# Kernel tuning notes

Measured on AMD Instinct MI355X. Metric: run time of the kernel, lower is better.

Reference implementation:

```python
import jax, jax.numpy as jnp
import numpy as np

N, M = 50000, 12
ORIG, NBR_F, AF = 92, 41, 64
B, NA = 500, 100
NCONV = 3
BN_EPS = 1e-5


def _batchnorm(x, g, b):
    # training-mode batchnorm over axis 0 (biased variance, like torch)
    mu = jnp.mean(x, axis=0)
    var = jnp.mean((x - mu) ** 2, axis=0)
    return (x - mu) * jax.lax.rsqrt(var + BN_EPS) * g + b


def _conv_layer(atom, nbr_fea, nbr_idx, W, bW, g1, b1, g2, b2):
    n, m = nbr_idx.shape
    atom_nbr = atom[nbr_idx]                                   # [N,M,AF] gather
    center = jnp.broadcast_to(atom[:, None, :], (n, m, AF))
    total = jnp.concatenate([center, atom_nbr, nbr_fea], axis=2)  # [N,M,2AF+NBR_F]
    gated = jnp.einsum('nmf,of->nmo', total, W) + bW              # [N,M,2AF]
    gated = _batchnorm(gated.reshape(-1, 2 * AF), g1, b1).reshape(n, m, 2 * AF)
    filt, core = gated[..., :AF], gated[..., AF:]
    summed = jnp.sum(jax.nn.sigmoid(filt) * jax.nn.softplus(core), axis=1)  # [N,AF]
    summed = _batchnorm(summed, g2, b2)
    return jax.nn.softplus(atom + summed)


def setup_inputs() -> dict:
    key = jax.random.key(0)
    ks = jax.random.split(key, 12)
    inp = {
        'atom_fea': jax.random.normal(ks[0], (N, ORIG), jnp.float32),
        'nbr_fea': jax.random.normal(ks[1], (N, M, NBR_F), jnp.float32),
        'nbr_fea_idx': jax.random.randint(ks[2], (N, M), 0, N, jnp.int32),
        'crystal_atom_idx': jnp.arange(B * NA, dtype=jnp.int32).reshape(B, NA),
        'mask': jnp.ones((ORIG,), jnp.float32),
        'emb_W': jax.random.normal(ks[3], (AF, ORIG), jnp.float32) * 0.05,
        'conv_W': jax.random.normal(ks[4], (NCONV, 2 * AF, 2 * AF + NBR_F), jnp.float32) * 0.05,
        'conv_b': jnp.zeros((NCONV, 2 * AF), jnp.float32),
        'bn1_g': jnp.ones((NCONV, 2 * AF), jnp.float32),
        'bn1_b': jnp.zeros((NCONV, 2 * AF), jnp.float32),
        'bn2_g': jnp.ones((NCONV, AF), jnp.float32),
        'bn2_b': jnp.zeros((NCONV, AF), jnp.float32),
        'fc1_W': jax.random.normal(ks[5], (AF, AF), jnp.float32) * 0.05,
        'fc1_b': jnp.zeros((AF,), jnp.float32),
        'fc2_W': jax.random.normal(ks[6], (AF, AF), jnp.float32) * 0.05,
        'fc2_b': jnp.zeros((AF,), jnp.float32),
        'out_W': jax.random.normal(ks[7], (1, AF), jnp.float32) * 0.05,
        'out_b': jnp.zeros((1,), jnp.float32),
    }
    return inp


def reference(atom_fea, nbr_fea, nbr_fea_idx, crystal_atom_idx, mask, emb_W,
              conv_W, conv_b, bn1_g, bn1_b, bn2_g, bn2_b,
              fc1_W, fc1_b, fc2_W, fc2_b, out_W, out_b):
    x = atom_fea * mask                      # learned input mask
    atom_mask_feature = x
    h = x @ emb_W.T                          # embedding, no bias -> [N,AF]
    for i in range(NCONV):
        h = _conv_layer(h, nbr_fea, nbr_fea_idx, conv_W[i], conv_b[i],
                        bn1_g[i], bn1_b[i], bn2_g[i], bn2_b[i])
    g = h[crystal_atom_idx]                  # [B,NA,AF]
    norm = jnp.sqrt(jnp.sum(g * g, axis=-1, keepdims=True))
    g = g / jnp.maximum(norm, 1e-12)         # F.normalize p=2
    pooled = jnp.mean(g, axis=1)             # [B,AF]
    z = jax.nn.softplus(pooled @ fc1_W.T + fc1_b)
    z = jax.nn.softplus(z @ fc2_W.T + fc2_b)
    props = z @ out_W.T + out_b              # [B,1]
    return props, atom_mask_feature
```

## Files before the change

kernel.cpp:

```cpp
#include <hip/hip_runtime.h>
#include <hip/hip_bf16.h>
#include <stdint.h>

#define NN      50000
#define MMN     12
#define NMROWS  600000
#define ORIGF   92
#define NBRF    41
#define AFD     64
#define GCH     128
#define KTOT    169
#define BBC     500
#define NAA     100
#define BN_EPS  1e-5f
#define GROWS   96

typedef unsigned short u16;
typedef __attribute__((ext_vector_type(8))) short bf16x8;
typedef __attribute__((ext_vector_type(4))) float f32x4;

__device__ __forceinline__ float b2f(u16 u) {
    union { uint32_t i; float f; } v; v.i = ((uint32_t)u) << 16; return v.f;
}
__device__ __forceinline__ float hi2f(uint32_t p) {
    union { uint32_t i; float f; } v; v.i = p & 0xffff0000u; return v.f;
}
__device__ __forceinline__ u16 f2b(float f) {
    __hip_bfloat16 h = __float2bfloat16(f);
    return *(u16*)&h;
}
__device__ __forceinline__ float sp_f(float x) {
    return fmaxf(x, 0.f) + __logf(1.f + __expf(-fabsf(x)));
}
__device__ __forceinline__ float sigm_f(float x) {
    return __builtin_amdgcn_rcpf(1.f + __expf(-x));
}

__global__ void k_mask(const float* __restrict__ atom, const float* __restrict__ mask,
                       float* __restrict__ dout) {
    int i = blockIdx.x * blockDim.x + threadIdx.x;
    int stride = gridDim.x * blockDim.x;
    for (; i < NN * ORIGF; i += stride) {
        int k = i % ORIGF;
        dout[BBC + i] = atom[i] * mask[k];
    }
}

__global__ __launch_bounds__(256, 2) void k_emb(const float* __restrict__ atom,
                                                const float* __restrict__ mask,
                                                const float* __restrict__ embW,
                                                u16* __restrict__ h) {
    __shared__ float xs[4 * 96];
    int lane = threadIdx.x & 63;
    int w = threadIdx.x >> 6;
    float wr[ORIGF];
#pragma unroll
    for (int k = 0; k < ORIGF; ++k) wr[k] = embW[lane * ORIGF + k];
    float m1 = mask[lane];
    float m2 = (lane < ORIGF - 64) ? mask[64 + lane] : 0.f;
    for (int base = blockIdx.x * 4; base < NN; base += gridDim.x * 4) {
        int n = base + w;
        xs[w * 96 + lane] = atom[(size_t)n * ORIGF + lane] * m1;
        if (lane < ORIGF - 64)
            xs[w * 96 + 64 + lane] = atom[(size_t)n * ORIGF + 64 + lane] * m2;
        __syncthreads();
        float acc = 0.f;
#pragma unroll
        for (int k4 = 0; k4 < ORIGF / 4; ++k4) {
            float4 f = *(const float4*)&xs[w * 96 + 4 * k4];
            acc += f.x * wr[4*k4] + f.y * wr[4*k4+1] + f.z * wr[4*k4+2] + f.w * wr[4*k4+3];
        }
        h[(size_t)n * AFD + lane] = f2b(acc);
        __syncthreads();
    }
}

__global__ __launch_bounds__(256, 2) void k_cn(const u16* __restrict__ h,
                                               const float* __restrict__ convW,
                                               uint32_t* __restrict__ C32) {
    __shared__ float xs[2 * AFD];
    int lane = threadIdx.x & 63;
    int w = threadIdx.x >> 6;
    int half = w & 1;
    int sub = w >> 1;
    int koff = half * AFD;
    float wa[AFD], wb[AFD];
#pragma unroll
    for (int k = 0; k < AFD; ++k) {
        wa[k] = convW[lane * KTOT + koff + k];
        wb[k] = convW[(lane + 64) * KTOT + koff + k];
    }
    for (int base = blockIdx.x * 2; base < NN; base += gridDim.x * 2) {
        int n = base + sub;
        if (half == 0) xs[sub * AFD + lane] = b2f(h[(size_t)n * AFD + lane]);
        __syncthreads();
        float aa = 0.f, ab = 0.f;
#pragma unroll
        for (int k4 = 0; k4 < AFD / 4; ++k4) {
            float4 f = *(const float4*)&xs[sub * AFD + 4 * k4];
            aa += f.x * wa[4*k4] + f.y * wa[4*k4+1] + f.z * wa[4*k4+2] + f.w * wa[4*k4+3];
            ab += f.x * wb[4*k4] + f.y * wb[4*k4+1] + f.z * wb[4*k4+2] + f.w * wb[4*k4+3];
        }
        C32[(size_t)n * 128 + half * 64 + lane] = (uint32_t)f2b(aa) | ((uint32_t)f2b(ab) << 16);
        __syncthreads();
    }
}

__device__ __forceinline__ void stage_nbrf(const float* nbrf, int r0, float* fs) {
    const float4* src = (const float4*)(nbrf + (size_t)r0 * NBRF);
    for (int t = threadIdx.x; t < (GROWS * NBRF) / 4; t += 256) {
        float4 f = src[t];
        float vals[4] = {f.x, f.y, f.z, f.w};
#pragma unroll
        for (int j = 0; j < 4; ++j) {
            int e = t * 4 + j;
            int row = e / NBRF;
            int k = e - row * NBRF;
            fs[row * 44 + k] = vals[j];
        }
    }
}

template<bool STORE>
__global__ __launch_bounds__(256, 4) void k_gs4(
    const uint32_t* __restrict__ C32, const float* __restrict__ nbrf,
    const int* __restrict__ nbridx, const float* __restrict__ convW,
    const float* __restrict__ convb, float* __restrict__ stats,
    uint32_t* __restrict__ gated32)
{
    __shared__ __align__(16) u16 As[GROWS * 56];
    __shared__ uint32_t C2s[GROWS * 65];
    __shared__ uint32_t C1s[8 * 65];
    const int tid  = threadIdx.x;
    const int lane = tid & 63;
    const int w    = tid >> 6;
    const int lr   = lane & 15;
    const int lg   = lane >> 4;
    const int r0    = blockIdx.x * GROWS;
    const int nbase = blockIdx.x * (GROWS / MMN);
    const int rowb  = w * 24;

    uint32_t c2v[12];
#pragma unroll
    for (int rr = 0; rr < 12; ++rr) {
        int j = nbridx[r0 + rowb + rr];
        c2v[rr] = C32[(size_t)j * 128 + 64 + lane];
    }
    uint32_t c1v[2];
#pragma unroll
    for (int q = 0; q < 2; ++q) {
        int e = tid + q * 256;
        c1v[q] = C32[(size_t)(nbase + (e >> 6)) * 128 + (e & 63)];
    }
    const float4* src4 = (const float4*)(nbrf + (size_t)r0 * NBRF);
#pragma unroll
    for (int it = 0; it < 4; ++it) {
        int t = tid + it * 256;
        if (it < 3 || t < 984) {
            float4 f = src4[t];
            float vals[4] = {f.x, f.y, f.z, f.w};
#pragma unroll
            for (int jj = 0; jj < 4; ++jj) {
                int e = t * 4 + jj;
                int row = e / NBRF;
                int k = e - row * NBRF;
                As[row * 56 + k] = f2b(vals[jj]);
            }
        }
    }
#pragma unroll
    for (int rr = 0; rr < 12; ++rr) C2s[(rowb + rr) * 65 + lane] = c2v[rr];
#pragma unroll
    for (int rr = 0; rr < 12; ++rr) {
        int j = nbridx[r0 + rowb + 12 + rr];
        c2v[rr] = C32[(size_t)j * 128 + 64 + lane];
    }
#pragma unroll
    for (int q = 0; q < 2; ++q) {
        int e = tid + q * 256;
        C1s[(e >> 6) * 65 + (e & 63)] = c1v[q];
    }
#pragma unroll
    for (int it = 0; it < 6; ++it) {
        int e = tid + it * 256;
        if (it < 5 || e < 1440) {
            int row = e / 15;
            int k = 41 + (e - row * 15);
            As[row * 56 + k] = (k == 41) ? (u16)0x3F80 : (u16)0;
        }
    }
    const int chlo = w * 16 + lr;
    const int chhi = chlo + 64;
    const float* wlo = convW + (size_t)chlo * KTOT + 128;
    const float* whi = convW + (size_t)chhi * KTOT + 128;
    bf16x8 bl0, bh0;
    bf16x8 bl1 = {0,0,0,0,0,0,0,0}, bh1 = {0,0,0,0,0,0,0,0};
#pragma unroll
    for (int e = 0; e < 8; ++e) {
        bl0[e] = (short)f2b(wlo[8 * lg + e]);
        bh0[e] = (short)f2b(whi[8 * lg + e]);
    }
    if (lg == 0) {
#pragma unroll
        for (int e = 0; e < 8; ++e) {
            bl1[e] = (short)f2b(wlo[32 + e]);
            bh1[e] = (short)f2b(whi[32 + e]);
        }
    } else if (lg == 1) {
        bl1[0] = (short)f2b(wlo[40]); bl1[1] = (short)f2b(convb[chlo]);
        bh1[0] = (short)f2b(whi[40]); bh1[1] = (short)f2b(convb[chhi]);
    }
#pragma unroll
    for (int rr = 0; rr < 12; ++rr) C2s[(rowb + 12 + rr) * 65 + lane] = c2v[rr];
    __syncthreads();

    f32x4 acc[6][2];
    const f32x4 z = {0.f, 0.f, 0.f, 0.f};
    const bf16x8 zb = {0,0,0,0,0,0,0,0};
#pragma unroll
    for (int mt = 0; mt < 6; ++mt) {
        const u16* ap = &As[(mt * 16 + lr) * 56 + 8 * lg];
        bf16x8 a0 = *(const bf16x8*)ap;
        bf16x8 a1 = zb;
        if (lg < 3) a1 = *(const bf16x8*)(ap + 32);
        acc[mt][0] = __builtin_amdgcn_mfma_f32_16x16x32_bf16(a1, bl1,
                     __builtin_amdgcn_mfma_f32_16x16x32_bf16(a0, bl0, z, 0, 0, 0), 0, 0, 0);
        acc[mt][1] = __builtin_amdgcn_mfma_f32_16x16x32_bf16(a1, bh1,
                     __builtin_amdgcn_mfma_f32_16x16x32_bf16(a0, bh0, z, 0, 0, 0), 0, 0, 0);
    }

    const int word = w * 16 + lr;
    float slo = 0.f, qlo = 0.f, shi = 0.f, qhi = 0.f;
#pragma unroll
    for (int mt = 0; mt < 6; ++mt) {
#pragma unroll
        for (int rg = 0; rg < 4; ++rg) {
            int row = mt * 16 + 4 * lg + rg;
            uint32_t p1 = C1s[(row / MMN) * 65 + word];
            uint32_t p2 = C2s[row * 65 + word];
            float glo = acc[mt][0][rg] + b2f((u16)p1) + b2f((u16)p2);
            float ghi = acc[mt][1][rg] + hi2f(p1) + hi2f(p2);
            if (STORE) {
                gated32[(size_t)(r0 + row) * 64 + word] =
                    (uint32_t)f2b(glo) | ((uint32_t)f2b(ghi) << 16);
            }
            slo += glo; qlo = fmaf(glo, glo, qlo);
            shi += ghi; qhi = fmaf(ghi, ghi, qhi);
        }
    }
    slo += __shfl_xor(slo, 16, 64); slo += __shfl_xor(slo, 32, 64);
    qlo += __shfl_xor(qlo, 16, 64); qlo += __shfl_xor(qlo, 32, 64);
    shi += __shfl_xor(shi, 16, 64); shi += __shfl_xor(shi, 32, 64);
    qhi += __shfl_xor(qhi, 16, 64); qhi += __shfl_xor(qhi, 32, 64);
    if (lane < 16) {
        atomicAdd(&stats[word], slo);
        atomicAdd(&stats[128 + word], qlo);
        atomicAdd(&stats[64 + word], shi);
        atomicAdd(&stats[128 + 64 + word], qhi);
    }
}

__global__ void k_fin(float* __restrict__ stats, const float* __restrict__ gg,
                      const float* __restrict__ bb, int nch, float invcnt,
                      int sumoff, int sqoff, int scoff, int shoff) {
    int c = threadIdx.x;
    if (c < nch) {
        float mean = stats[sumoff + c] * invcnt;
        float var  = fmaxf(stats[sqoff + c] * invcnt - mean * mean, 0.f);
        float sc   = gg[c] * rsqrtf(var + BN_EPS);
        stats[scoff + c] = sc;
        stats[shoff + c] = bb[c] - mean * sc;
    }
}

__global__ __launch_bounds__(256) void k_acts(
    const uint32_t* __restrict__ gated32, float* __restrict__ stats,
    u16* __restrict__ summed)
{
    __shared__ float red[4][64][2];
    int lane = threadIdx.x & 63;
    int w = threadIdx.x >> 6;
    float sa = stats[384 + lane],      ba = stats[512 + lane];
    float sb = stats[384 + 64 + lane], bb = stats[512 + 64 + lane];
    int wave = blockIdx.x * 4 + w, nw = gridDim.x * 4;
    float s2 = 0.f, q2 = 0.f;
    for (int n = wave; n < NN; n += nw) {
        const uint32_t* gr = gated32 + (size_t)n * MMN * 64;
        float s = 0.f;
#pragma unroll
        for (int m = 0; m < MMN; ++m) {
            uint32_t p = gr[m * 64 + lane];
            float f1 = b2f((u16)p) * sa + ba;
            float cc = hi2f(p) * sb + bb;
            s += sigm_f(f1) * sp_f(cc);
        }
        summed[(size_t)n * AFD + lane] = f2b(s);
        s2 += s; q2 += s * s;
    }
    red[w][lane][0] = s2; red[w][lane][1] = q2;
    __syncthreads();
    if (threadIdx.x < 64) {
        int c = threadIdx.x;
        float a = 0, b = 0;
#pragma unroll
        for (int ww = 0; ww < 4; ++ww) { a += red[ww][c][0]; b += red[ww][c][1]; }
        atomicAdd(&stats[256 + c], a);
        atomicAdd(&stats[320 + c], b);
    }
}

__device__ __forceinline__ void edge_dot(const float* fr, const float* wfa,
                                         const float* wfb, float& aa, float& ab) {
#pragma unroll
    for (int k4 = 0; k4 < 10; ++k4) {
        float4 f = *(const float4*)&fr[4 * k4];
        aa += f.x * wfa[4*k4] + f.y * wfa[4*k4+1] + f.z * wfa[4*k4+2] + f.w * wfa[4*k4+3];
        ab += f.x * wfb[4*k4] + f.y * wfb[4*k4+1] + f.z * wfb[4*k4+2] + f.w * wfb[4*k4+3];
    }
    aa += fr[40] * wfa[40];
    ab += fr[40] * wfb[40];
}

__global__ __launch_bounds__(256) void k_act(
    const uint32_t* __restrict__ C32, const float* __restrict__ nbrf,
    const int* __restrict__ nbridx, const float* __restrict__ convW,
    const float* __restrict__ convb, float* __restrict__ stats,
    u16* __restrict__ summed)
{
    __shared__ float fs[GROWS * 44];
    __shared__ float red[4][64][2];
    int lane = threadIdx.x & 63;
    int w = threadIdx.x >> 6;
    int r0 = blockIdx.x * GROWS;
    stage_nbrf(nbrf, r0, fs);
    float wfa[NBRF], wfb[NBRF];
#pragma unroll
    for (int k = 0; k < NBRF; ++k) {
        wfa[k] = convW[lane * KTOT + 128 + k];
        wfb[k] = convW[(lane + 64) * KTOT + 128 + k];
    }
    float biasa = convb[lane], biasb = convb[64 + lane];
    float sa = stats[384 + lane],      ba = stats[512 + lane];
    float sb = stats[384 + 64 + lane], bb = stats[512 + 64 + lane];
    __syncthreads();
    float s2 = 0.f, q2 = 0.f;
    float s = 0.f;
    float c1a = 0.f, c1b = 0.f;
    for (int rr = 0; rr < 24; ++rr) {
        int rl = w * 24 + rr;
        int r = r0 + rl;
        if ((rr % MMN) == 0) {
            int n = r / MMN;
            uint32_t p1 = C32[(size_t)n * 128 + lane];
            c1a = b2f((u16)p1); c1b = b2f((u16)(p1 >> 16));
            s = 0.f;
        }
        int j = nbridx[r];
        uint32_t p2 = C32[(size_t)j * 128 + 64 + lane];
        float aa = c1a + b2f((u16)p2) + biasa;
        float ab = c1b + b2f((u16)(p2 >> 16)) + biasb;
        edge_dot(&fs[rl * 44], wfa, wfb, aa, ab);
        float f1 = aa * sa + ba;
        float cc = ab * sb + bb;
        s += sigm_f(f1) * sp_f(cc);
        if ((rr % MMN) == MMN - 1) {
            int n = r / MMN;
            summed[(size_t)n * AFD + lane] = f2b(s);
            s2 += s; q2 += s * s;
        }
    }
    red[w][lane][0] = s2; red[w][lane][1] = q2;
    __syncthreads();
    if (threadIdx.x < 64) {
        int c = threadIdx.x;
        float a = 0, b = 0;
#pragma unroll
        for (int ww = 0; ww < 4; ++ww) { a += red[ww][c][0]; b += red[ww][c][1]; }
        atomicAdd(&stats[256 + c], a);
        atomicAdd(&stats[320 + c], b);
    }
}

__global__ void k_update(u16* __restrict__ h, const u16* __restrict__ summed,
                         const float* __restrict__ stats) {
    int i = blockIdx.x * blockDim.x + threadIdx.x;
    int st = gridDim.x * blockDim.x;
    int c = threadIdx.x & 63;
    float sc = stats[640 + c], shf = stats[704 + c];
    for (; i < NN * AFD; i += st) {
        float x = b2f(h[i]) + b2f(summed[i]) * sc + shf;
        h[i] = f2b(sp_f(x));
    }
}

__global__ __launch_bounds__(256) void k_pool(const u16* __restrict__ h,
                                              const int* __restrict__ cry,
                                              float* __restrict__ pooled) {
    __shared__ float red[4][64];
    int lane = threadIdx.x & 63, w = threadIdx.x >> 6;
    int b = blockIdx.x;
    float acc = 0.f;
    for (int a = w; a < NAA; a += 4) {
        int idx = cry[b * NAA + a];
        float v = b2f(h[(size_t)idx * AFD + lane]);
        float s2 = v * v;
#pragma unroll
        for (int o = 32; o > 0; o >>= 1) s2 += __shfl_xor(s2, o, 64);
        acc += v / fmaxf(sqrtf(s2), 1e-12f);
    }
    red[w][lane] = acc;
    __syncthreads();
    if (threadIdx.x < 64) {
        float s = red[0][threadIdx.x] + red[1][threadIdx.x] +
                  red[2][threadIdx.x] + red[3][threadIdx.x];
        pooled[b * AFD + threadIdx.x] = s * (1.f / NAA);
    }
}

__global__ __launch_bounds__(64) void k_head(const float* __restrict__ pooled,
    const float* __restrict__ fc1W, const float* __restrict__ fc1b,
    const float* __restrict__ fc2W, const float* __restrict__ fc2b,
    const float* __restrict__ outW, const float* __restrict__ outb,
    float* __restrict__ props) {
    __shared__ float W1[64 * 65], W2[64 * 65], zbuf[64], pbuf[64];
    int l = threadIdx.x;
    for (int e = l; e < 64 * 64; e += 64) {
        int o = e >> 6, k = e & 63;
        W1[o * 65 + k] = fc1W[e];
        W2[o * 65 + k] = fc2W[e];
    }
    int b = blockIdx.x;
    pbuf[l] = pooled[b * AFD + l];
    __syncthreads();
    float acc = fc1b[l];
#pragma unroll
    for (int k = 0; k < 64; ++k) acc += pbuf[k] * W1[l * 65 + k];
    zbuf[l] = sp_f(acc);
    __syncthreads();
    acc = fc2b[l];
#pragma unroll
    for (int k = 0; k < 64; ++k) acc += zbuf[k] * W2[l * 65 + k];
    float v = sp_f(acc) * outW[l];
#pragma unroll
    for (int o = 32; o > 0; o >>= 1) v += __shfl_xor(v, o, 64);
    if (l == 0) props[b] = v + outb[0];
}

extern "C" void kernel_launch(void* const* d_in, const int* in_sizes, int n_in,
                              void* d_out, int out_size, void* d_ws, size_t ws_size,
                              hipStream_t stream) {
    const float* atom  = (const float*)d_in[0];
    const float* nbrf  = (const float*)d_in[1];
    const int* nbridx  = (const int*)d_in[2];
    const int* cry     = (const int*)d_in[3];
    const float* mask  = (const float*)d_in[4];
    const float* embW  = (const float*)d_in[5];
    const float* convW = (const float*)d_in[6];
    const float* convb = (const float*)d_in[7];
    const float* bn1g  = (const float*)d_in[8];
    const float* bn1b  = (const float*)d_in[9];
    const float* bn2g  = (const float*)d_in[10];
    const float* bn2b  = (const float*)d_in[11];
    const float* fc1W  = (const float*)d_in[12];
    const float* fc1b  = (const float*)d_in[13];
    const float* fc2W  = (const float*)d_in[14];
    const float* fc2b  = (const float*)d_in[15];
    const float* outW  = (const float*)d_in[16];
    const float* outb  = (const float*)d_in[17];

    char* ws = (char*)d_ws;
    float* stats    = (float*)ws;
    float* pooled   = (float*)(ws + 4096);
    u16*   h        = (u16*)(ws + (1u << 20));
    u16*   summed   = (u16*)(ws + (8u << 20));
    uint32_t* C32   = (uint32_t*)(ws + (16u << 20));
    uint32_t* gated32 = (uint32_t*)(ws + (48u << 20));
    const bool bigws = ws_size >= (size_t)(48u << 20) + 153600000u;

    float* out_props = (float*)d_out;

    k_mask<<<2048, 256, 0, stream>>>(atom, mask, (float*)d_out);
    k_emb<<<512, 256, 0, stream>>>(atom, mask, embW, h);
    for (int i = 0; i < 3; ++i) {
        hipMemsetAsync(stats, 0, 384 * sizeof(float), stream);
        k_cn<<<1024, 256, 0, stream>>>(h, convW + (size_t)i * GCH * KTOT, C32);
        if (bigws)
            k_gs4<true><<<NMROWS / GROWS, 256, 0, stream>>>(C32, nbrf, nbridx,
                convW + (size_t)i * GCH * KTOT, convb + (size_t)i * GCH, stats, gated32);
        else
            k_gs4<false><<<NMROWS / GROWS, 256, 0, stream>>>(C32, nbrf, nbridx,
                convW + (size_t)i * GCH * KTOT, convb + (size_t)i * GCH, stats, gated32);
        k_fin<<<1, 128, 0, stream>>>(stats, bn1g + (size_t)i * GCH, bn1b + (size_t)i * GCH,
                                     128, 1.f / NMROWS, 0, 128, 384, 512);
        if (bigws)
            k_acts<<<1024, 256, 0, stream>>>(gated32, stats, summed);
        else
            k_act<<<NMROWS / GROWS, 256, 0, stream>>>(C32, nbrf, nbridx,
                convW + (size_t)i * GCH * KTOT, convb + (size_t)i * GCH, stats, summed);
        k_fin<<<1, 128, 0, stream>>>(stats, bn2g + (size_t)i * AFD, bn2b + (size_t)i * AFD,
                                     64, 1.f / NN, 256, 320, 640, 704);
        k_update<<<1024, 256, 0, stream>>>(h, summed, stats);
    }
    k_pool<<<BBC, 256, 0, stream>>>(h, cry, pooled);
    k_head<<<BBC, 64, 0, stream>>>(pooled, fc1W, fc1b, fc2W, fc2b, outW, outb, out_props);
}
```

Baseline: 1.040 ms.

## Transpose gathered neighbor tiles in LDS and batch all gathers up front

The gather+GEMM kernel now loads one neighbor index per lane and broadcasts it with shuffles. It issues all 24 neighbor-row gathers and the nbr_fea float4 loads before any LDS writes, so more loads are in flight at once. The gathered center and neighbor tiles are stored transposed in LDS, which lets the epilogue read four consecutive rows with one 128-bit load. The A tile row stride shrinks from 56 to 48 to save LDS, but the larger register footprint (24 gathered words plus staged float4s) may raise register pressure at 4 blocks per CU, and the transposed stride of 100 words may cause bank conflicts on the stores.

Measured after the change: 1.041 ms. Within noise of the previous version (+0.1%).

```diff
diff --git a/kernel.cpp b/kernel.cpp
--- a/kernel.cpp
+++ b/kernel.cpp
@@ -18,6 +18,7 @@
 typedef unsigned short u16;
 typedef __attribute__((ext_vector_type(8))) short bf16x8;
 typedef __attribute__((ext_vector_type(4))) float f32x4;
+typedef __attribute__((ext_vector_type(4))) unsigned int u32x4;
 
 __device__ __forceinline__ float b2f(u16 u) {
     union { uint32_t i; float f; } v; v.i = ((uint32_t)u) << 16; return v.f;
@@ -122,15 +123,15 @@
 }
 
 template<bool STORE>
-__global__ __launch_bounds__(256, 4) void k_gs4(
+__global__ __launch_bounds__(256, 4) void k_gs5(
     const uint32_t* __restrict__ C32, const float* __restrict__ nbrf,
     const int* __restrict__ nbridx, const float* __restrict__ convW,
     const float* __restrict__ convb, float* __restrict__ stats,
     uint32_t* __restrict__ gated32)
 {
-    __shared__ __align__(16) u16 As[GROWS * 56];
-    __shared__ uint32_t C2s[GROWS * 65];
-    __shared__ uint32_t C1s[8 * 65];
+    __shared__ __align__(16) u16 As[GROWS * 48];
+    __shared__ __align__(16) uint32_t C2T[64 * 100];
+    __shared__ __align__(16) uint32_t C1T[64 * 12];
     const int tid  = threadIdx.x;
     const int lane = tid & 63;
     const int w    = tid >> 6;
@@ -140,12 +141,7 @@
     const int nbase = blockIdx.x * (GROWS / MMN);
     const int rowb  = w * 24;
 
-    uint32_t c2v[12];
-#pragma unroll
-    for (int rr = 0; rr < 12; ++rr) {
-        int j = nbridx[r0 + rowb + rr];
-        c2v[rr] = C32[(size_t)j * 128 + 64 + lane];
-    }
+    int jv = nbridx[r0 + rowb + (lane < 24 ? lane : 0)];
     uint32_t c1v[2];
 #pragma unroll
     for (int q = 0; q < 2; ++q) {
@@ -153,41 +149,11 @@
         c1v[q] = C32[(size_t)(nbase + (e >> 6)) * 128 + (e & 63)];
     }
     const float4* src4 = (const float4*)(nbrf + (size_t)r0 * NBRF);
+    float4 af[4];
 #pragma unroll
     for (int it = 0; it < 4; ++it) {
         int t = tid + it * 256;
-        if (it < 3 || t < 984) {
-            float4 f = src4[t];
-            float vals[4] = {f.x, f.y, f.z, f.w};
-#pragma unroll
-            for (int jj = 0; jj < 4; ++jj) {
-                int e = t * 4 + jj;
-                int row = e / NBRF;
-                int k = e - row * NBRF;
-                As[row * 56 + k] = f2b(vals[jj]);
-            }
-        }
-    }
-#pragma unroll
-    for (int rr = 0; rr < 12; ++rr) C2s[(rowb + rr) * 65 + lane] = c2v[rr];
-#pragma unroll
-    for (int rr = 0; rr < 12; ++rr) {
-        int j = nbridx[r0 + rowb + 12 + rr];
-        c2v[rr] = C32[(size_t)j * 128 + 64 + lane];
-    }
-#pragma unroll
-    for (int q = 0; q < 2; ++q) {
-        int e = tid + q * 256;
-        C1s[(e >> 6) * 65 + (e & 63)] = c1v[q];
-    }
-#pragma unroll
-    for (int it = 0; it < 6; ++it) {
-        int e = tid + it * 256;
-        if (it < 5 || e < 1440) {
-            int row = e / 15;
-            int k = 41 + (e - row * 15);
-            As[row * 56 + k] = (k == 41) ? (u16)0x3F80 : (u16)0;
-        }
+        if (it < 3 || t < 984) af[it] = src4[t];
     }
     const int chlo = w * 16 + lr;
     const int chhi = chlo + 64;
@@ -210,8 +176,39 @@
         bl1[0] = (short)f2b(wlo[40]); bl1[1] = (short)f2b(convb[chlo]);
         bh1[0] = (short)f2b(whi[40]); bh1[1] = (short)f2b(convb[chhi]);
     }
-#pragma unroll
-    for (int rr = 0; rr < 12; ++rr) C2s[(rowb + 12 + rr) * 65 + lane] = c2v[rr];
+    uint32_t c2v[24];
+#pragma unroll
+    for (int rr = 0; rr < 24; ++rr) {
+        int j = __shfl(jv, rr, 64);
+        c2v[rr] = C32[(size_t)j * 128 + 64 + lane];
+    }
+#pragma unroll
+    for (int it = 0; it < 4; ++it) {
+        int t = tid + it * 256;
+        if (it < 3 || t < 984) {
+            float4 f = af[it];
+            float vals[4] = {f.x, f.y, f.z, f.w};
+#pragma unroll
+            for (int jj = 0; jj < 4; ++jj) {
+                int e = t * 4 + jj;
+                int row = e / NBRF;
+                int k = e - row * NBRF;
+                As[row * 48 + k] = f2b(vals[jj]);
+            }
+        }
+    }
+    for (int e = tid; e < 672; e += 256) {
+        int row = e / 7;
+        int k = 41 + (e - row * 7);
+        As[row * 48 + k] = (k == 41) ? (u16)0x3F80 : (u16)0;
+    }
+#pragma unroll
+    for (int q = 0; q < 2; ++q) {
+        int e = tid + q * 256;
+        C1T[(e & 63) * 12 + (e >> 6)] = c1v[q];
+    }
+#pragma unroll
+    for (int rr = 0; rr < 24; ++rr) C2T[lane * 100 + rowb + rr] = c2v[rr];
     __syncthreads();
 
     f32x4 acc[6][2];
@@ -219,10 +216,10 @@
     const bf16x8 zb = {0,0,0,0,0,0,0,0};
 #pragma unroll
     for (int mt = 0; mt < 6; ++mt) {
-        const u16* ap = &As[(mt * 16 + lr) * 56 + 8 * lg];
+        const u16* ap = &As[(mt * 16 + lr) * 48 + 8 * lg];
         bf16x8 a0 = *(const bf16x8*)ap;
         bf16x8 a1 = zb;
-        if (lg < 3) a1 = *(const bf16x8*)(ap + 32);
+        if (lg < 2) a1 = *(const bf16x8*)(ap + 32);
         acc[mt][0] = __builtin_amdgcn_mfma_f32_16x16x32_bf16(a1, bl1,
                      __builtin_amdgcn_mfma_f32_16x16x32_bf16(a0, bl0, z, 0, 0, 0), 0, 0, 0);
         acc[mt][1] = __builtin_amdgcn_mfma_f32_16x16x32_bf16(a1, bh1,
@@ -233,13 +230,13 @@
     float slo = 0.f, qlo = 0.f, shi = 0.f, qhi = 0.f;
 #pragma unroll
     for (int mt = 0; mt < 6; ++mt) {
+        u32x4 p2 = *(const u32x4*)&C2T[word * 100 + mt * 16 + 4 * lg];
 #pragma unroll
         for (int rg = 0; rg < 4; ++rg) {
             int row = mt * 16 + 4 * lg + rg;
-            uint32_t p1 = C1s[(row / MMN) * 65 + word];
-            uint32_t p2 = C2s[row * 65 + word];
-            float glo = acc[mt][0][rg] + b2f((u16)p1) + b2f((u16)p2);
-            float ghi = acc[mt][1][rg] + hi2f(p1) + hi2f(p2);
+            uint32_t p1 = C1T[word * 12 + row / MMN];
+            float glo = acc[mt][0][rg] + b2f((u16)p1) + b2f((u16)p2[rg]);
+            float ghi = acc[mt][1][rg] + hi2f(p1) + hi2f(p2[rg]);
             if (STORE) {
                 gated32[(size_t)(r0 + row) * 64 + word] =
                     (uint32_t)f2b(glo) | ((uint32_t)f2b(ghi) << 16);
@@ -485,10 +482,10 @@
         hipMemsetAsync(stats, 0, 384 * sizeof(float), stream);
         k_cn<<<1024, 256, 0, stream>>>(h, convW + (size_t)i * GCH * KTOT, C32);
         if (bigws)
-            k_gs4<true><<<NMROWS / GROWS, 256, 0, stream>>>(C32, nbrf, nbridx,
+            k_gs5<true><<<NMROWS / GROWS, 256, 0, stream>>>(C32, nbrf, nbridx,
                 convW + (size_t)i * GCH * KTOT, convb + (size_t)i * GCH, stats, gated32);
         else
-            k_gs4<false><<<NMROWS / GROWS, 256, 0, stream>>>(C32, nbrf, nbridx,
+            k_gs5<false><<<NMROWS / GROWS, 256, 0, stream>>>(C32, nbrf, nbridx,
                 convW + (size_t)i * GCH * KTOT, convb + (size_t)i * GCH, stats, gated32);
         k_fin<<<1, 128, 0, stream>>>(stats, bn1g + (size_t)i * GCH, bn1b + (size_t)i * GCH,
                                      128, 1.f / NMROWS, 0, 128, 384, 512);
```
